# Optimization experiments

Hardware: AMD Instinct MI355X
Metric: run time of the kernel (lower is better)

Reference implementation:

```python
import jax, jax.numpy as jnp
import numpy as np

N = 8192
IN_F = 256
OUT_F = 128
E = 262144
NEG = -9e15


def setup_inputs() -> dict:
    key = jax.random.key(0)
    ks = jax.random.split(key, 12)
    glorot = lambda k, shp: jax.random.uniform(k, shp, jnp.float32,
                                               -jnp.sqrt(6.0 / (shp[0] + shp[1])),
                                               jnp.sqrt(6.0 / (shp[0] + shp[1])))
    return {
        "h_context": jax.random.normal(ks[0], (N, IN_F), jnp.float32),
        "h_structure": jax.random.normal(ks[1], (N, IN_F), jnp.float32),
        "edge_index": jax.random.randint(ks[2], (2, E), 0, N, jnp.int64),
        "Wc_w": glorot(ks[3], (OUT_F, IN_F)),
        "Wc_b": jnp.zeros((OUT_F,), jnp.float32),
        "Ws_w": glorot(ks[4], (OUT_F, IN_F)),
        "Ws_b": jnp.zeros((OUT_F,), jnp.float32),
        "ac_w": glorot(ks[5], (1, 2 * OUT_F)),
        "as_w": glorot(ks[6], (1, 2 * OUT_F)),
        "Ws_coff": jax.random.normal(ks[7], (1, 1), jnp.float32) * 1.414,
        "Wc_coff": jax.random.normal(ks[8], (1, 1), jnp.float32) * 1.414,
    }


def _pair_scores(h, a_w):
    # GAT trick: score[i,j] = leaky_relu(a1 . h[i] + a2 . h[j])
    F_out = h.shape[1]
    s_src = h @ a_w[0, :F_out]   # [N]
    s_dst = h @ a_w[0, F_out:]   # [N]
    return jax.nn.leaky_relu(s_src[:, None] + s_dst[None, :], 0.01)  # [N, N]


def reference(h_context, h_structure, edge_index, Wc_w, Wc_b, Ws_w, Ws_b,
              ac_w, as_w, Ws_coff, Wc_coff):
    hc = h_context @ Wc_w.T + Wc_b                      # [N, F]
    alpha_c = _pair_scores(hc, ac_w)                    # [N, N]
    hs = jax.nn.softmax(h_structure, axis=1) @ Ws_w.T + Ws_b
    alpha_s = _pair_scores(hs, as_w)                    # [N, N]
    alpha = jnp.abs(Ws_coff[0, 0]) * alpha_c + jnp.abs(Wc_coff[0, 0]) * alpha_s
    n = h_structure.shape[0]
    adj = jnp.zeros((n, n), bool).at[edge_index[0], edge_index[1]].set(True)
    attention = jnp.where(adj, alpha, NEG)
    attention = jax.nn.softmax(attention, axis=1)
    # dropout omitted (eval mode / deterministic reference)
    return attention @ hc
```

## Files before the change

kernel.cpp:

```cpp
#include <hip/hip_runtime.h>
#include <math.h>

#define N_NODES 8192
#define IN_FEAT 256
#define OUT_FEAT 128
#define CAP 128
#define M_TILE 32
#define NF_BLOCKS 512

typedef unsigned long long u64;
typedef float v4f __attribute__((ext_vector_type(4)));
typedef short s8v __attribute__((ext_vector_type(8)));
typedef short s4v __attribute__((ext_vector_type(4)));

__device__ __forceinline__ float wred_sum_b(float v) {
    #pragma unroll
    for (int o = 32; o > 0; o >>= 1) v += __shfl_xor(v, o, 64);
    return v;
}
__device__ __forceinline__ float wred_max_b(float v) {
    #pragma unroll
    for (int o = 32; o > 0; o >>= 1) v = fmaxf(v, __shfl_xor(v, o, 64));
    return v;
}

__device__ __forceinline__ void bsplit(float x, unsigned short& hi, unsigned short& lo) {
    unsigned int xb = __float_as_uint(x);
    hi = (unsigned short)(xb >> 16);
    float lof = x - __uint_as_float(xb & 0xFFFF0000u);
    lo = (unsigned short)(__float_as_uint(lof) >> 16);
}

__global__ __launch_bounds__(256) void prep(
    const float* __restrict__ Wc, const float* __restrict__ Ws,
    int* __restrict__ cnt,
    unsigned short* __restrict__ cfrag, unsigned short* __restrict__ sfrag)
{
    int tid = blockIdx.x * 256 + threadIdx.x;
    if (tid < 2048) ((int4*)cnt)[tid] = make_int4(0, 0, 0, 0);

    int mat = tid >> 13;
    int f = tid & 8191;
    int lnf = f & 63;
    int sel = (f >> 6) & 3;
    int ks  = (f >> 8) & 7;
    int wv  = (f >> 11) & 3;
    int row = (wv << 5) + ((sel >> 1) << 4) + (lnf & 15);
    int part = sel & 1;
    int k0 = (ks << 5) + ((lnf >> 4) << 3);
    const float* src = (mat ? Ws : Wc) + row * IN_FEAT + k0;
    short tmp[8];
    #pragma unroll
    for (int j = 0; j < 8; j++) {
        float x = src[j];
        unsigned int xb = __float_as_uint(x);
        if (part == 0) tmp[j] = (short)(xb >> 16);
        else {
            float lof = x - __uint_as_float(xb & 0xFFFF0000u);
            tmp[j] = (short)(__float_as_uint(lof) >> 16);
        }
    }
    unsigned short* dst = (mat ? sfrag : cfrag) + (size_t)f * 8;
    *(s8v*)dst = *(const s8v*)tmp;
}

__global__ __launch_bounds__(256, 4) void node_feats(
    const float* __restrict__ hctx, const float* __restrict__ hstr,
    const unsigned short* __restrict__ cfrag, const unsigned short* __restrict__ sfrag,
    const float* __restrict__ Wcb, const float* __restrict__ Wsb,
    const float* __restrict__ acw, const float* __restrict__ asw,
    const int* __restrict__ ei, int E,
    int* __restrict__ cnt, unsigned short* __restrict__ adj,
    float* __restrict__ hc,
    float* __restrict__ csrc, float* __restrict__ ssrc,
    float* __restrict__ dpack)
{
    __shared__ unsigned short aH[M_TILE][264], aL[M_TILE][264];
    __shared__ float invsh[M_TILE];
    float (*hT)[132] = (float(*)[132])&aH[0][0];

    const int t = threadIdx.x;
    const int w = t >> 6, ln = t & 63;
    const int is_struct = (blockIdx.x >= 256);
    const int b = blockIdx.x & 255;
    const int r0 = b * M_TILE;

    {
        int pv = ei[2 * (ln & 31) + 1];
        u64 nz = __ballot(pv != 0);
        if (nz == 0) {
            for (int e2 = (blockIdx.x * 256 + t) * 2; e2 < E; e2 += NF_BLOCKS * 512) {
                int4 sv = *(const int4*)(ei + 2 * e2);
                int4 dv = *(const int4*)(ei + 2 * E + 2 * e2);
                if ((unsigned)sv.x < N_NODES && (unsigned)dv.x < N_NODES) {
                    int idx = atomicAdd(&cnt[sv.x], 1);
                    if (idx < CAP) adj[(size_t)sv.x * CAP + idx] = (unsigned short)dv.x;
                }
                if (e2 + 1 < E && (unsigned)sv.z < N_NODES && (unsigned)dv.z < N_NODES) {
                    int idx = atomicAdd(&cnt[sv.z], 1);
                    if (idx < CAP) adj[(size_t)sv.z * CAP + idx] = (unsigned short)dv.z;
                }
            }
        } else {
            for (int e = blockIdx.x * 256 + t; e < E; e += NF_BLOCKS * 256) {
                int s = ei[e], d = ei[E + e];
                if ((unsigned)s < N_NODES && (unsigned)d < N_NODES) {
                    int idx = atomicAdd(&cnt[s], 1);
                    if (idx < CAP) adj[(size_t)s * CAP + idx] = (unsigned short)d;
                }
            }
        }
    }

    if (!is_struct) {
        #pragma unroll
        for (int j = 0; j < 8; j++) {
            int c = t + 256 * j;
            int r = c >> 6;
            int k = (c & 63) * 4;
            const float4 x = *(const float4*)(hctx + (size_t)(r0 + r) * IN_FEAT + k);
            unsigned short h0, h1, h2, h3, l0, l1, l2, l3;
            bsplit(x.x, h0, l0); bsplit(x.y, h1, l1);
            bsplit(x.z, h2, l2); bsplit(x.w, h3, l3);
            s4v hv = { (short)h0, (short)h1, (short)h2, (short)h3 };
            s4v lv = { (short)l0, (short)l1, (short)l2, (short)l3 };
            *(s4v*)&aH[r][k] = hv;
            *(s4v*)&aL[r][k] = lv;
        }
    } else {
        #pragma unroll
        for (int rr = 0; rr < 8; rr++) {
            int r = w * 8 + rr;
            const float* srow = hstr + (size_t)(r0 + r) * IN_FEAT;
            float x0 = srow[ln], x1 = srow[ln + 64], x2 = srow[ln + 128], x3 = srow[ln + 192];
            float mx = wred_max_b(fmaxf(fmaxf(x0, x1), fmaxf(x2, x3)));
            float e0 = __expf(x0 - mx), e1 = __expf(x1 - mx);
            float e2 = __expf(x2 - mx), e3 = __expf(x3 - mx);
            float s = wred_sum_b(e0 + e1 + e2 + e3);
            if (ln == 0) invsh[r] = 1.0f / s;
            unsigned short h, l;
            bsplit(e0, h, l); aH[r][ln]       = h; aL[r][ln]       = l;
            bsplit(e1, h, l); aH[r][ln + 64]  = h; aL[r][ln + 64]  = l;
            bsplit(e2, h, l); aH[r][ln + 128] = h; aL[r][ln + 128] = l;
            bsplit(e3, h, l); aH[r][ln + 192] = h; aL[r][ln + 192] = l;
        }
    }
    __syncthreads();

    const int m = ln & 15, q = ln >> 4;
    const unsigned short* frag = is_struct ? sfrag : cfrag;

    v4f a00 = {0.f,0.f,0.f,0.f}, a01 = {0.f,0.f,0.f,0.f};
    v4f a10 = {0.f,0.f,0.f,0.f}, a11 = {0.f,0.f,0.f,0.f};

    #pragma unroll 2
    for (int ks = 0; ks < 8; ks++) {
        const int k0 = ks * 32 + q * 8;
        const s8v* base = (const s8v*)frag + ((w * 8 + ks) * 4) * 64 + ln;
        s8v bh0 = base[0];
        s8v bl0 = base[64];
        s8v bh1 = base[128];
        s8v bl1 = base[192];
        s8v ah0 = *(const s8v*)&aH[m][k0];
        s8v al0 = *(const s8v*)&aL[m][k0];
        s8v ah1 = *(const s8v*)&aH[m + 16][k0];
        s8v al1 = *(const s8v*)&aL[m + 16][k0];
        a00 = __builtin_amdgcn_mfma_f32_16x16x32_bf16(al0, bh0, a00, 0, 0, 0);
        a00 = __builtin_amdgcn_mfma_f32_16x16x32_bf16(ah0, bl0, a00, 0, 0, 0);
        a00 = __builtin_amdgcn_mfma_f32_16x16x32_bf16(ah0, bh0, a00, 0, 0, 0);
        a01 = __builtin_amdgcn_mfma_f32_16x16x32_bf16(al0, bh1, a01, 0, 0, 0);
        a01 = __builtin_amdgcn_mfma_f32_16x16x32_bf16(ah0, bl1, a01, 0, 0, 0);
        a01 = __builtin_amdgcn_mfma_f32_16x16x32_bf16(ah0, bh1, a01, 0, 0, 0);
        a10 = __builtin_amdgcn_mfma_f32_16x16x32_bf16(al1, bh0, a10, 0, 0, 0);
        a10 = __builtin_amdgcn_mfma_f32_16x16x32_bf16(ah1, bl0, a10, 0, 0, 0);
        a10 = __builtin_amdgcn_mfma_f32_16x16x32_bf16(ah1, bh0, a10, 0, 0, 0);
        a11 = __builtin_amdgcn_mfma_f32_16x16x32_bf16(al1, bh1, a11, 0, 0, 0);
        a11 = __builtin_amdgcn_mfma_f32_16x16x32_bf16(ah1, bl1, a11, 0, 0, 0);
        a11 = __builtin_amdgcn_mfma_f32_16x16x32_bf16(ah1, bh1, a11, 0, 0, 0);
    }
    __syncthreads();

    const int nA = (w << 5) + m, nB = nA + 16;
    if (!is_struct) {
        const float bA = Wcb[nA], bB = Wcb[nB];
        #pragma unroll
        for (int p = 0; p < 4; p++) {
            int row = q * 4 + p;
            hT[row][nA]      = a00[p] + bA;
            hT[row][nB]      = a01[p] + bB;
            hT[row + 16][nA] = a10[p] + bA;
            hT[row + 16][nB] = a11[p] + bB;
        }
        __syncthreads();

        #pragma unroll
        for (int j = 0; j < 16; j++) {
            int f = t + 256 * j;
            int r = f >> 7, c = f & 127;
            hc[(size_t)(r0 + r) * OUT_FEAT + c] = hT[r][c];
        }
        float a0 = acw[ln], a0b = acw[ln + 64], a1 = acw[128 + ln], a1b = acw[192 + ln];
        #pragma unroll
        for (int rr = 0; rr < 8; rr++) {
            int r = w * 8 + rr;
            float c0 = hT[r][ln], c1 = hT[r][ln + 64];
            float v0 = wred_sum_b(c0 * a0 + c1 * a0b);
            float v1 = wred_sum_b(c0 * a1 + c1 * a1b);
            if (ln == 0) { csrc[r0 + r] = v0; dpack[2 * (r0 + r)] = v1; }
        }
    } else {
        const float bA = Wsb[nA], bB = Wsb[nB];
        float iv0[4], iv1[4];
        #pragma unroll
        for (int p = 0; p < 4; p++) { iv0[p] = invsh[q * 4 + p]; iv1[p] = invsh[q * 4 + p + 16]; }
        #pragma unroll
        for (int p = 0; p < 4; p++) {
            int row = q * 4 + p;
            hT[row][nA]      = a00[p] * iv0[p] + bA;
            hT[row][nB]      = a01[p] * iv0[p] + bB;
            hT[row + 16][nA] = a10[p] * iv1[p] + bA;
            hT[row + 16][nB] = a11[p] * iv1[p] + bB;
        }
        __syncthreads();

        float b0 = asw[ln], b0b = asw[ln + 64], b1 = asw[128 + ln], b1b = asw[192 + ln];
        #pragma unroll
        for (int rr = 0; rr < 8; rr++) {
            int r = w * 8 + rr;
            float s0 = hT[r][ln], s1 = hT[r][ln + 64];
            float v2 = wred_sum_b(s0 * b0 + s1 * b0b);
            float v3 = wred_sum_b(s0 * b1 + s1 * b1b);
            if (ln == 0) { ssrc[r0 + r] = v2; dpack[2 * (r0 + r) + 1] = v3; }
        }
    }
}

__global__ __launch_bounds__(256) void attn(
    const int* __restrict__ cntArr, const unsigned short* __restrict__ adj,
    const float* __restrict__ hc,
    const float* __restrict__ csrc, const float* __restrict__ ssrc,
    const float2* __restrict__ dpack,
    const float* __restrict__ wscoff, const float* __restrict__ wccoff,
    float* __restrict__ out)
{
    __shared__ float2       jp[4][CAP];
    __shared__ unsigned int bm[4][256];

    const int w  = threadIdx.x >> 6;
    const int ln = threadIdx.x & 63;
    const int i  = blockIdx.x * 4 + w;

    const float wS = fabsf(wscoff[0]);
    const float wC = fabsf(wccoff[0]);
    const float cs = csrc[i], ss = ssrc[i];

    int cnt = cntArr[i];
    if (cnt > CAP) cnt = CAP;

    if (cnt == 0) {
        float2 acc = {0.f, 0.f};
        const float2* hc2f = (const float2*)hc;
        for (int j = 0; j < N_NODES; j++) {
            float2 h2 = hc2f[(size_t)j * 64 + ln];
            acc.x += h2.x; acc.y += h2.y;
        }
        float2 o2 = { acc.x / (float)N_NODES, acc.y / (float)N_NODES };
        *(float2*)(out + (size_t)i * OUT_FEAT + 2 * ln) = o2;
        return;
    }

    bm[w][ln]       = 0u;
    bm[w][ln + 64]  = 0u;
    bm[w][ln + 128] = 0u;
    bm[w][ln + 192] = 0u;

    const unsigned short* row = adj + (size_t)i * CAP;
    int j0 = (ln < cnt)      ? (int)row[ln]      : -1;
    int j1 = (64 + ln < cnt) ? (int)row[64 + ln] : -1;
    __threadfence_block();

    bool keep0 = false, keep1 = false;
    if (j0 >= 0) {
        unsigned int bit = 1u << (j0 & 31);
        keep0 = !(atomicOr(&bm[w][j0 >> 5], bit) & bit);
    }
    if (j1 >= 0) {
        unsigned int bit = 1u << (j1 & 31);
        keep1 = !(atomicOr(&bm[w][j1 >> 5], bit) & bit);
    }

    float al0 = -3e38f, al1 = -3e38f;
    if (keep0) {
        float2 d  = dpack[j0];
        float ac  = cs + d.x;
        float as_ = ss + d.y;
        ac  = (ac  > 0.0f) ? ac  : 0.01f * ac;
        as_ = (as_ > 0.0f) ? as_ : 0.01f * as_;
        al0 = wS * ac + wC * as_;
    }
    if (keep1) {
        float2 d  = dpack[j1];
        float ac  = cs + d.x;
        float as_ = ss + d.y;
        ac  = (ac  > 0.0f) ? ac  : 0.01f * ac;
        as_ = (as_ > 0.0f) ? as_ : 0.01f * as_;
        al1 = wS * ac + wC * as_;
    }

    float m = wred_max_b(fmaxf(al0, al1));
    float p0 = __expf(al0 - m);
    float p1 = __expf(al1 - m);
    float s = wred_sum_b(p0 + p1);
    float inv = 1.0f / s;

    jp[w][ln]      = make_float2(p0, __int_as_float(j0));
    jp[w][64 + ln] = make_float2(p1, __int_as_float(j1));
    __threadfence_block();

    const int half = ln >> 5;
    const int c4   = ln & 31;
    const float4* hc4 = (const float4*)hc;
    float4 acc = {0.f, 0.f, 0.f, 0.f};

    int k = 0;
    for (; k + 8 <= cnt; k += 8) {
        float4 hx[4];
        float  px[4];
        #pragma unroll
        for (int u = 0; u < 4; u++) {
            int idx = k + 2 * u + half;
            float2 e = jp[w][idx];
            px[u] = e.x;
            hx[u] = hc4[__float_as_int(e.y) * 32 + c4];
        }
        #pragma unroll
        for (int u = 0; u < 4; u++) {
            acc.x += px[u] * hx[u].x;
            acc.y += px[u] * hx[u].y;
            acc.z += px[u] * hx[u].z;
            acc.w += px[u] * hx[u].w;
        }
    }
    for (; k < cnt; k += 2) {
        int idx = k + half;
        float2 e = jp[w][(idx < cnt) ? idx : 0];
        float p = (idx < cnt) ? e.x : 0.0f;
        float4 h = hc4[__float_as_int(e.y) * 32 + c4];
        acc.x += p * h.x; acc.y += p * h.y;
        acc.z += p * h.z; acc.w += p * h.w;
    }

    acc.x += __shfl_xor(acc.x, 32, 64);
    acc.y += __shfl_xor(acc.y, 32, 64);
    acc.z += __shfl_xor(acc.z, 32, 64);
    acc.w += __shfl_xor(acc.w, 32, 64);
    if (half == 0) {
        float4 o4 = { acc.x * inv, acc.y * inv, acc.z * inv, acc.w * inv };
        *(float4*)(out + (size_t)i * OUT_FEAT + 4 * c4) = o4;
    }
}

extern "C" void kernel_launch(void* const* d_in, const int* in_sizes, int n_in,
                              void* d_out, int out_size, void* d_ws, size_t ws_size,
                              hipStream_t stream)
{
    const float* hctx = (const float*)d_in[0];
    const float* hstr = (const float*)d_in[1];
    const int*   ei   = (const int*)d_in[2];
    const float* Wc   = (const float*)d_in[3];
    const float* Wcb  = (const float*)d_in[4];
    const float* Ws   = (const float*)d_in[5];
    const float* Wsb  = (const float*)d_in[6];
    const float* acw  = (const float*)d_in[7];
    const float* asw  = (const float*)d_in[8];
    const float* wsco = (const float*)d_in[9];
    const float* wcco = (const float*)d_in[10];
    float* out = (float*)d_out;

    const int n2 = in_sizes[2];
    const int E  = (n2 == 4 * 262144) ? 262144 : n2 / 2;

    char* ws = (char*)d_ws;
    size_t off = 0;
    float* hc    = (float*)(ws + off); off += (size_t)N_NODES * OUT_FEAT * sizeof(float);
    float* csrc  = (float*)(ws + off); off += (size_t)N_NODES * sizeof(float);
    float* ssrc  = (float*)(ws + off); off += (size_t)N_NODES * sizeof(float);
    float* dpack = (float*)(ws + off); off += (size_t)N_NODES * 2 * sizeof(float);
    off = (off + 255) & ~(size_t)255;
    int* cnt = (int*)(ws + off);      off += (size_t)N_NODES * sizeof(int);
    unsigned short* adj = (unsigned short*)(ws + off); off += (size_t)N_NODES * CAP * sizeof(unsigned short);
    unsigned short* cfrag = (unsigned short*)(ws + off); off += (size_t)8192 * 8 * sizeof(unsigned short);
    unsigned short* sfrag = (unsigned short*)(ws + off); off += (size_t)8192 * 8 * sizeof(unsigned short);

    prep<<<64, 256, 0, stream>>>(Wc, Ws, cnt, cfrag, sfrag);
    node_feats<<<NF_BLOCKS, 256, 0, stream>>>(hctx, hstr, cfrag, sfrag, Wcb, Wsb,
                                              acw, asw, ei, E, cnt, adj,
                                              hc, csrc, ssrc, dpack);
    attn<<<N_NODES / 4, 256, 0, stream>>>(cnt, adj, hc, csrc, ssrc, (const float2*)dpack,
                                          wsco, wcco, out);
}
```

Before: 116.9 us.

## Fuse prep, node features and attention into one cooperative kernel with grid syncs

```diff
diff --git a/kernel.cpp b/kernel.cpp
--- a/kernel.cpp
+++ b/kernel.cpp
@@ -1,12 +1,14 @@
 #include <hip/hip_runtime.h>
+#include <hip/hip_cooperative_groups.h>
 #include <math.h>
+
+namespace cg = cooperative_groups;
 
 #define N_NODES 8192
 #define IN_FEAT 256
 #define OUT_FEAT 128
 #define CAP 128
 #define M_TILE 32
-#define NF_BLOCKS 512
 
 typedef unsigned long long u64;
 typedef float v4f __attribute__((ext_vector_type(4)));
@@ -31,65 +33,64 @@
     lo = (unsigned short)(__float_as_uint(lof) >> 16);
 }
 
-__global__ __launch_bounds__(256) void prep(
+__device__ __forceinline__ void dev_prep(int tid,
     const float* __restrict__ Wc, const float* __restrict__ Ws,
     int* __restrict__ cnt,
     unsigned short* __restrict__ cfrag, unsigned short* __restrict__ sfrag)
 {
-    int tid = blockIdx.x * 256 + threadIdx.x;
     if (tid < 2048) ((int4*)cnt)[tid] = make_int4(0, 0, 0, 0);
-
-    int mat = tid >> 13;
-    int f = tid & 8191;
-    int lnf = f & 63;
-    int sel = (f >> 6) & 3;
-    int ks  = (f >> 8) & 7;
-    int wv  = (f >> 11) & 3;
-    int row = (wv << 5) + ((sel >> 1) << 4) + (lnf & 15);
-    int part = sel & 1;
-    int k0 = (ks << 5) + ((lnf >> 4) << 3);
-    const float* src = (mat ? Ws : Wc) + row * IN_FEAT + k0;
-    short tmp[8];
-    #pragma unroll
-    for (int j = 0; j < 8; j++) {
-        float x = src[j];
-        unsigned int xb = __float_as_uint(x);
-        if (part == 0) tmp[j] = (short)(xb >> 16);
-        else {
-            float lof = x - __uint_as_float(xb & 0xFFFF0000u);
-            tmp[j] = (short)(__float_as_uint(lof) >> 16);
-        }
-    }
-    unsigned short* dst = (mat ? sfrag : cfrag) + (size_t)f * 8;
-    *(s8v*)dst = *(const s8v*)tmp;
-}
-
-__global__ __launch_bounds__(256, 4) void node_feats(
+    if (tid < 16384) {
+        int mat = tid >> 13;
+        int f = tid & 8191;
+        int lnf = f & 63;
+        int sel = (f >> 6) & 3;
+        int ks  = (f >> 8) & 7;
+        int wv  = (f >> 11) & 3;
+        int row = (wv << 5) + ((sel >> 1) << 4) + (lnf & 15);
+        int part = sel & 1;
+        int k0 = (ks << 5) + ((lnf >> 4) << 3);
+        const float* src = (mat ? Ws : Wc) + row * IN_FEAT + k0;
+        short tmp[8];
+        #pragma unroll
+        for (int j = 0; j < 8; j++) {
+            float x = src[j];
+            unsigned int xb = __float_as_uint(x);
+            if (part == 0) tmp[j] = (short)(xb >> 16);
+            else {
+                float lof = x - __uint_as_float(xb & 0xFFFF0000u);
+                tmp[j] = (short)(__float_as_uint(lof) >> 16);
+            }
+        }
+        unsigned short* dst = (mat ? sfrag : cfrag) + (size_t)f * 8;
+        *(s8v*)dst = *(const s8v*)tmp;
+    }
+}
+
+__device__ __forceinline__ void dev_nf(
     const float* __restrict__ hctx, const float* __restrict__ hstr,
     const unsigned short* __restrict__ cfrag, const unsigned short* __restrict__ sfrag,
     const float* __restrict__ Wcb, const float* __restrict__ Wsb,
     const float* __restrict__ acw, const float* __restrict__ asw,
     const int* __restrict__ ei, int E,
     int* __restrict__ cnt, unsigned short* __restrict__ adj,
-    float* __restrict__ hc,
-    float* __restrict__ csrc, float* __restrict__ ssrc,
-    float* __restrict__ dpack)
-{
-    __shared__ unsigned short aH[M_TILE][264], aL[M_TILE][264];
+    float* __restrict__ hc, float* __restrict__ csrc, float* __restrict__ ssrc,
+    float* __restrict__ dpack, int blk, int t)
+{
+    __shared__ __align__(16) unsigned short aH[M_TILE][264], aL[M_TILE][264];
     __shared__ float invsh[M_TILE];
     float (*hT)[132] = (float(*)[132])&aH[0][0];
 
-    const int t = threadIdx.x;
     const int w = t >> 6, ln = t & 63;
-    const int is_struct = (blockIdx.x >= 256);
-    const int b = blockIdx.x & 255;
+    const int is_struct = (blk >= 256);
+    const int b = blk & 255;
     const int r0 = b * M_TILE;
 
-    {
+    if (!is_struct) {
         int pv = ei[2 * (ln & 31) + 1];
         u64 nz = __ballot(pv != 0);
+        int ctid = blk * 512 + t;
         if (nz == 0) {
-            for (int e2 = (blockIdx.x * 256 + t) * 2; e2 < E; e2 += NF_BLOCKS * 512) {
+            for (int e2 = ctid * 2; e2 < E; e2 += 262144) {
                 int4 sv = *(const int4*)(ei + 2 * e2);
                 int4 dv = *(const int4*)(ei + 2 * E + 2 * e2);
                 if ((unsigned)sv.x < N_NODES && (unsigned)dv.x < N_NODES) {
@@ -102,7 +103,7 @@
                 }
             }
         } else {
-            for (int e = blockIdx.x * 256 + t; e < E; e += NF_BLOCKS * 256) {
+            for (int e = ctid; e < E; e += 131072) {
                 int s = ei[e], d = ei[E + e];
                 if ((unsigned)s < N_NODES && (unsigned)d < N_NODES) {
                     int idx = atomicAdd(&cnt[s], 1);
@@ -110,12 +111,9 @@
                 }
             }
         }
-    }
-
-    if (!is_struct) {
-        #pragma unroll
-        for (int j = 0; j < 8; j++) {
-            int c = t + 256 * j;
+        #pragma unroll
+        for (int j = 0; j < 4; j++) {
+            int c = t + 512 * j;
             int r = c >> 6;
             int k = (c & 63) * 4;
             const float4 x = *(const float4*)(hctx + (size_t)(r0 + r) * IN_FEAT + k);
@@ -129,8 +127,8 @@
         }
     } else {
         #pragma unroll
-        for (int rr = 0; rr < 8; rr++) {
-            int r = w * 8 + rr;
+        for (int rr = 0; rr < 4; rr++) {
+            int r = w * 4 + rr;
             const float* srow = hstr + (size_t)(r0 + r) * IN_FEAT;
             float x0 = srow[ln], x1 = srow[ln + 64], x2 = srow[ln + 128], x3 = srow[ln + 192];
             float mx = wred_max_b(fmaxf(fmaxf(x0, x1), fmaxf(x2, x3)));
@@ -148,85 +146,71 @@
     __syncthreads();
 
     const int m = ln & 15, q = ln >> 4;
+    const int w4 = w >> 1, pair = w & 1;
     const unsigned short* frag = is_struct ? sfrag : cfrag;
 
-    v4f a00 = {0.f,0.f,0.f,0.f}, a01 = {0.f,0.f,0.f,0.f};
-    v4f a10 = {0.f,0.f,0.f,0.f}, a11 = {0.f,0.f,0.f,0.f};
+    v4f a00 = {0.f,0.f,0.f,0.f}, a10 = {0.f,0.f,0.f,0.f};
 
     #pragma unroll 2
     for (int ks = 0; ks < 8; ks++) {
         const int k0 = ks * 32 + q * 8;
-        const s8v* base = (const s8v*)frag + ((w * 8 + ks) * 4) * 64 + ln;
-        s8v bh0 = base[0];
-        s8v bl0 = base[64];
-        s8v bh1 = base[128];
-        s8v bl1 = base[192];
+        const s8v* base = (const s8v*)frag + ((w4 * 8 + ks) * 4) * 64 + pair * 128 + ln;
+        s8v bh = base[0];
+        s8v bl = base[64];
         s8v ah0 = *(const s8v*)&aH[m][k0];
         s8v al0 = *(const s8v*)&aL[m][k0];
         s8v ah1 = *(const s8v*)&aH[m + 16][k0];
         s8v al1 = *(const s8v*)&aL[m + 16][k0];
-        a00 = __builtin_amdgcn_mfma_f32_16x16x32_bf16(al0, bh0, a00, 0, 0, 0);
-        a00 = __builtin_amdgcn_mfma_f32_16x16x32_bf16(ah0, bl0, a00, 0, 0, 0);
-        a00 = __builtin_amdgcn_mfma_f32_16x16x32_bf16(ah0, bh0, a00, 0, 0, 0);
-        a01 = __builtin_amdgcn_mfma_f32_16x16x32_bf16(al0, bh1, a01, 0, 0, 0);
-        a01 = __builtin_amdgcn_mfma_f32_16x16x32_bf16(ah0, bl1, a01, 0, 0, 0);
-        a01 = __builtin_amdgcn_mfma_f32_16x16x32_bf16(ah0, bh1, a01, 0, 0, 0);
-        a10 = __builtin_amdgcn_mfma_f32_16x16x32_bf16(al1, bh0, a10, 0, 0, 0);
-        a10 = __builtin_amdgcn_mfma_f32_16x16x32_bf16(ah1, bl0, a10, 0, 0, 0);
-        a10 = __builtin_amdgcn_mfma_f32_16x16x32_bf16(ah1, bh0, a10, 0, 0, 0);
-        a11 = __builtin_amdgcn_mfma_f32_16x16x32_bf16(al1, bh1, a11, 0, 0, 0);
-        a11 = __builtin_amdgcn_mfma_f32_16x16x32_bf16(ah1, bl1, a11, 0, 0, 0);
-        a11 = __builtin_amdgcn_mfma_f32_16x16x32_bf16(ah1, bh1, a11, 0, 0, 0);
+        a00 = __builtin_amdgcn_mfma_f32_16x16x32_bf16(al0, bh, a00, 0, 0, 0);
+        a00 = __builtin_amdgcn_mfma_f32_16x16x32_bf16(ah0, bl, a00, 0, 0, 0);
+        a00 = __builtin_amdgcn_mfma_f32_16x16x32_bf16(ah0, bh, a00, 0, 0, 0);
+        a10 = __builtin_amdgcn_mfma_f32_16x16x32_bf16(al1, bh, a10, 0, 0, 0);
+        a10 = __builtin_amdgcn_mfma_f32_16x16x32_bf16(ah1, bl, a10, 0, 0, 0);
+        a10 = __builtin_amdgcn_mfma_f32_16x16x32_bf16(ah1, bh, a10, 0, 0, 0);
     }
     __syncthreads();
 
-    const int nA = (w << 5) + m, nB = nA + 16;
+    const int nc = (w << 4) + m;
     if (!is_struct) {
-        const float bA = Wcb[nA], bB = Wcb[nB];
+        const float bC = Wcb[nc];
         #pragma unroll
         for (int p = 0; p < 4; p++) {
             int row = q * 4 + p;
-            hT[row][nA]      = a00[p] + bA;
-            hT[row][nB]      = a01[p] + bB;
-            hT[row + 16][nA] = a10[p] + bA;
-            hT[row + 16][nB] = a11[p] + bB;
+            hT[row][nc]      = a00[p] + bC;
+            hT[row + 16][nc] = a10[p] + bC;
         }
         __syncthreads();
-
-        #pragma unroll
-        for (int j = 0; j < 16; j++) {
-            int f = t + 256 * j;
-            int r = f >> 7, c = f & 127;
-            hc[(size_t)(r0 + r) * OUT_FEAT + c] = hT[r][c];
+        #pragma unroll
+        for (int j = 0; j < 8; j++) {
+            int f = t + 512 * j;
+            int r = f >> 7, c2 = f & 127;
+            hc[(size_t)(r0 + r) * OUT_FEAT + c2] = hT[r][c2];
         }
         float a0 = acw[ln], a0b = acw[ln + 64], a1 = acw[128 + ln], a1b = acw[192 + ln];
         #pragma unroll
-        for (int rr = 0; rr < 8; rr++) {
-            int r = w * 8 + rr;
+        for (int rr = 0; rr < 4; rr++) {
+            int r = w * 4 + rr;
             float c0 = hT[r][ln], c1 = hT[r][ln + 64];
             float v0 = wred_sum_b(c0 * a0 + c1 * a0b);
             float v1 = wred_sum_b(c0 * a1 + c1 * a1b);
             if (ln == 0) { csrc[r0 + r] = v0; dpack[2 * (r0 + r)] = v1; }
         }
     } else {
-        const float bA = Wsb[nA], bB = Wsb[nB];
+        const float bS = Wsb[nc];
         float iv0[4], iv1[4];
         #pragma unroll
         for (int p = 0; p < 4; p++) { iv0[p] = invsh[q * 4 + p]; iv1[p] = invsh[q * 4 + p + 16]; }
         #pragma unroll
         for (int p = 0; p < 4; p++) {
             int row = q * 4 + p;
-            hT[row][nA]      = a00[p] * iv0[p] + bA;
-            hT[row][nB]      = a01[p] * iv0[p] + bB;
-            hT[row + 16][nA] = a10[p] * iv1[p] + bA;
-            hT[row + 16][nB] = a11[p] * iv1[p] + bB;
+            hT[row][nc]      = a00[p] * iv0[p] + bS;
+            hT[row + 16][nc] = a10[p] * iv1[p] + bS;
         }
         __syncthreads();
-
         float b0 = asw[ln], b0b = asw[ln + 64], b1 = asw[128 + ln], b1b = asw[192 + ln];
         #pragma unroll
-        for (int rr = 0; rr < 8; rr++) {
-            int r = w * 8 + rr;
+        for (int rr = 0; rr < 4; rr++) {
+            int r = w * 4 + rr;
             float s0 = hT[r][ln], s1 = hT[r][ln + 64];
             float v2 = wred_sum_b(s0 * b0 + s1 * b0b);
             float v3 = wred_sum_b(s0 * b1 + s1 * b1b);
@@ -235,25 +219,14 @@
     }
 }
 
-__global__ __launch_bounds__(256) void attn(
+__device__ __forceinline__ void dev_attn_row(int i, int ln,
+    float2* jp, unsigned int* bm,
     const int* __restrict__ cntArr, const unsigned short* __restrict__ adj,
-    const float* __restrict__ hc,
-    const float* __restrict__ csrc, const float* __restrict__ ssrc,
-    const float2* __restrict__ dpack,
-    const float* __restrict__ wscoff, const float* __restrict__ wccoff,
-    float* __restrict__ out)
-{
-    __shared__ float2       jp[4][CAP];
-    __shared__ unsigned int bm[4][256];
-
-    const int w  = threadIdx.x >> 6;
-    const int ln = threadIdx.x & 63;
-    const int i  = blockIdx.x * 4 + w;
-
-    const float wS = fabsf(wscoff[0]);
-    const float wC = fabsf(wccoff[0]);
+    const float* __restrict__ hc, const float* __restrict__ csrc,
+    const float* __restrict__ ssrc, const float2* __restrict__ dpack,
+    float wS, float wC, float* __restrict__ out)
+{
     const float cs = csrc[i], ss = ssrc[i];
-
     int cnt = cntArr[i];
     if (cnt > CAP) cnt = CAP;
 
@@ -269,10 +242,7 @@
         return;
     }
 
-    bm[w][ln]       = 0u;
-    bm[w][ln + 64]  = 0u;
-    bm[w][ln + 128] = 0u;
-    bm[w][ln + 192] = 0u;
+    bm[ln] = 0u; bm[ln + 64] = 0u; bm[ln + 128] = 0u; bm[ln + 192] = 0u;
 
     const unsigned short* row = adj + (size_t)i * CAP;
     int j0 = (ln < cnt)      ? (int)row[ln]      : -1;
@@ -282,11 +252,11 @@
     bool keep0 = false, keep1 = false;
     if (j0 >= 0) {
         unsigned int bit = 1u << (j0 & 31);
-        keep0 = !(atomicOr(&bm[w][j0 >> 5], bit) & bit);
+        keep0 = !(atomicOr(&bm[j0 >> 5], bit) & bit);
     }
     if (j1 >= 0) {
         unsigned int bit = 1u << (j1 & 31);
-        keep1 = !(atomicOr(&bm[w][j1 >> 5], bit) & bit);
+        keep1 = !(atomicOr(&bm[j1 >> 5], bit) & bit);
     }
 
     float al0 = -3e38f, al1 = -3e38f;
@@ -307,14 +277,14 @@
         al1 = wS * ac + wC * as_;
     }
 
-    float m = wred_max_b(fmaxf(al0, al1));
-    float p0 = __expf(al0 - m);
-    float p1 = __expf(al1 - m);
+    float mm = wred_max_b(fmaxf(al0, al1));
+    float p0 = __expf(al0 - mm);
+    float p1 = __expf(al1 - mm);
     float s = wred_sum_b(p0 + p1);
     float inv = 1.0f / s;
 
-    jp[w][ln]      = make_float2(p0, __int_as_float(j0));
-    jp[w][64 + ln] = make_float2(p1, __int_as_float(j1));
+    jp[ln]      = make_float2(p0, __int_as_float(j0));
+    jp[64 + ln] = make_float2(p1, __int_as_float(j1));
     __threadfence_block();
 
     const int half = ln >> 5;
@@ -329,7 +299,7 @@
         #pragma unroll
         for (int u = 0; u < 4; u++) {
             int idx = k + 2 * u + half;
-            float2 e = jp[w][idx];
+            float2 e = jp[idx];
             px[u] = e.x;
             hx[u] = hc4[__float_as_int(e.y) * 32 + c4];
         }
@@ -343,7 +313,7 @@
     }
     for (; k < cnt; k += 2) {
         int idx = k + half;
-        float2 e = jp[w][(idx < cnt) ? idx : 0];
+        float2 e = jp[(idx < cnt) ? idx : 0];
         float p = (idx < cnt) ? e.x : 0.0f;
         float4 h = hc4[__float_as_int(e.y) * 32 + c4];
         acc.x += p * h.x; acc.y += p * h.y;
@@ -358,6 +328,64 @@
         float4 o4 = { acc.x * inv, acc.y * inv, acc.z * inv, acc.w * inv };
         *(float4*)(out + (size_t)i * OUT_FEAT + 4 * c4) = o4;
     }
+}
+
+struct FA {
+    const float *hctx, *hstr, *Wc, *Ws, *Wcb, *Wsb, *acw, *asw;
+    const int *ei;
+    int E;
+    const float *wsco, *wcco;
+    int *cnt;
+    unsigned short *adj;
+    float *hc, *csrc, *ssrc, *dpack;
+    unsigned short *cfrag, *sfrag;
+    float *out;
+};
+
+__global__ __launch_bounds__(512, 4) void fused(FA a)
+{
+    const int t = threadIdx.x, blk = blockIdx.x;
+    dev_prep(blk * 512 + t, a.Wc, a.Ws, a.cnt, a.cfrag, a.sfrag);
+    cg::this_grid().sync();
+    dev_nf(a.hctx, a.hstr, a.cfrag, a.sfrag, a.Wcb, a.Wsb, a.acw, a.asw,
+           a.ei, a.E, a.cnt, a.adj, a.hc, a.csrc, a.ssrc, a.dpack, blk, t);
+    cg::this_grid().sync();
+
+    __shared__ __align__(16) float2 jpA[8][CAP];
+    __shared__ unsigned int bmA[8][256];
+    const int w = t >> 6, ln = t & 63;
+    const float wS  = fabsf(a.wsco[0]);
+    const float wCc = fabsf(a.wcco[0]);
+    dev_attn_row(blk * 16 + w * 2,     ln, &jpA[w][0], &bmA[w][0], a.cnt, a.adj,
+                 a.hc, a.csrc, a.ssrc, (const float2*)a.dpack, wS, wCc, a.out);
+    dev_attn_row(blk * 16 + w * 2 + 1, ln, &jpA[w][0], &bmA[w][0], a.cnt, a.adj,
+                 a.hc, a.csrc, a.ssrc, (const float2*)a.dpack, wS, wCc, a.out);
+}
+
+__global__ __launch_bounds__(256) void prep_k(
+    const float* __restrict__ Wc, const float* __restrict__ Ws,
+    int* __restrict__ cnt,
+    unsigned short* __restrict__ cfrag, unsigned short* __restrict__ sfrag)
+{
+    dev_prep(blockIdx.x * 256 + threadIdx.x, Wc, Ws, cnt, cfrag, sfrag);
+}
+
+__global__ __launch_bounds__(512, 4) void nf_k(FA a)
+{
+    dev_nf(a.hctx, a.hstr, a.cfrag, a.sfrag, a.Wcb, a.Wsb, a.acw, a.asw,
+           a.ei, a.E, a.cnt, a.adj, a.hc, a.csrc, a.ssrc, a.dpack,
+           blockIdx.x, threadIdx.x);
+}
+
+__global__ __launch_bounds__(256) void attn_k(FA a)
+{
+    __shared__ __align__(16) float2 jpA[4][CAP];
+    __shared__ unsigned int bmA[4][256];
+    const int w = threadIdx.x >> 6, ln = threadIdx.x & 63;
+    const float wS  = fabsf(a.wsco[0]);
+    const float wCc = fabsf(a.wcco[0]);
+    dev_attn_row(blockIdx.x * 4 + w, ln, &jpA[w][0], &bmA[w][0], a.cnt, a.adj,
+                 a.hc, a.csrc, a.ssrc, (const float2*)a.dpack, wS, wCc, a.out);
 }
 
 extern "C" void kernel_launch(void* const* d_in, const int* in_sizes, int n_in,
@@ -378,7 +406,7 @@
     float* out = (float*)d_out;
 
     const int n2 = in_sizes[2];
-    const int E  = (n2 == 4 * 262144) ? 262144 : n2 / 2;
+    int E = (n2 == 4 * 262144) ? 262144 : n2 / 2;
 
     char* ws = (char*)d_ws;
     size_t off = 0;
@@ -392,10 +420,20 @@
     unsigned short* cfrag = (unsigned short*)(ws + off); off += (size_t)8192 * 8 * sizeof(unsigned short);
     unsigned short* sfrag = (unsigned short*)(ws + off); off += (size_t)8192 * 8 * sizeof(unsigned short);
 
-    prep<<<64, 256, 0, stream>>>(Wc, Ws, cnt, cfrag, sfrag);
-    node_feats<<<NF_BLOCKS, 256, 0, stream>>>(hctx, hstr, cfrag, sfrag, Wcb, Wsb,
-                                              acw, asw, ei, E, cnt, adj,
-                                              hc, csrc, ssrc, dpack);
-    attn<<<N_NODES / 4, 256, 0, stream>>>(cnt, adj, hc, csrc, ssrc, (const float2*)dpack,
-                                          wsco, wcco, out);
-}
+    FA fa;
+    fa.hctx = hctx; fa.hstr = hstr; fa.Wc = Wc; fa.Ws = Ws;
+    fa.Wcb = Wcb; fa.Wsb = Wsb; fa.acw = acw; fa.asw = asw;
+    fa.ei = ei; fa.E = E; fa.wsco = wsco; fa.wcco = wcco;
+    fa.cnt = cnt; fa.adj = adj; fa.hc = hc; fa.csrc = csrc; fa.ssrc = ssrc;
+    fa.dpack = dpack; fa.cfrag = cfrag; fa.sfrag = sfrag; fa.out = out;
+
+    void* args[] = { (void*)&fa };
+    hipError_t ce = hipLaunchCooperativeKernel(fused, dim3(512), dim3(512),
+                                               args, 0, stream);
+    if (ce != hipSuccess) {
+        (void)hipGetLastError();
+        prep_k<<<64, 256, 0, stream>>>(Wc, Ws, cnt, cfrag, sfrag);
+        nf_k<<<512, 512, 0, stream>>>(fa);
+        attn_k<<<N_NODES / 4, 256, 0, stream>>>(fa);
+    }
+}
```

Measured after the change: 241.6 us. +106.8%, slower.

## Double node-feature block size and move edge scatter to context blocks only

Applied to the files above, without the earlier changes.

```diff
diff --git a/kernel.cpp b/kernel.cpp
--- a/kernel.cpp
+++ b/kernel.cpp
@@ -6,7 +6,6 @@
 #define OUT_FEAT 128
 #define CAP 128
 #define M_TILE 32
-#define NF_BLOCKS 512
 
 typedef unsigned long long u64;
 typedef float v4f __attribute__((ext_vector_type(4)));
@@ -31,7 +30,7 @@
     lo = (unsigned short)(__float_as_uint(lof) >> 16);
 }
 
-__global__ __launch_bounds__(256) void prep(
+__global__ __launch_bounds__(256) void prep_k(
     const float* __restrict__ Wc, const float* __restrict__ Ws,
     int* __restrict__ cnt,
     unsigned short* __restrict__ cfrag, unsigned short* __restrict__ sfrag)
@@ -64,32 +63,32 @@
     *(s8v*)dst = *(const s8v*)tmp;
 }
 
-__global__ __launch_bounds__(256, 4) void node_feats(
+__global__ __launch_bounds__(512, 4) void nf_k(
     const float* __restrict__ hctx, const float* __restrict__ hstr,
     const unsigned short* __restrict__ cfrag, const unsigned short* __restrict__ sfrag,
     const float* __restrict__ Wcb, const float* __restrict__ Wsb,
     const float* __restrict__ acw, const float* __restrict__ asw,
     const int* __restrict__ ei, int E,
     int* __restrict__ cnt, unsigned short* __restrict__ adj,
-    float* __restrict__ hc,
-    float* __restrict__ csrc, float* __restrict__ ssrc,
+    float* __restrict__ hc, float* __restrict__ csrc, float* __restrict__ ssrc,
     float* __restrict__ dpack)
 {
-    __shared__ unsigned short aH[M_TILE][264], aL[M_TILE][264];
+    __shared__ __align__(16) unsigned short aH[M_TILE][264], aL[M_TILE][264];
     __shared__ float invsh[M_TILE];
     float (*hT)[132] = (float(*)[132])&aH[0][0];
 
-    const int t = threadIdx.x;
+    const int t = threadIdx.x, blk = blockIdx.x;
     const int w = t >> 6, ln = t & 63;
-    const int is_struct = (blockIdx.x >= 256);
-    const int b = blockIdx.x & 255;
+    const int is_struct = (blk >= 256);
+    const int b = blk & 255;
     const int r0 = b * M_TILE;
 
-    {
+    if (!is_struct) {
         int pv = ei[2 * (ln & 31) + 1];
         u64 nz = __ballot(pv != 0);
+        int ctid = blk * 512 + t;
         if (nz == 0) {
-            for (int e2 = (blockIdx.x * 256 + t) * 2; e2 < E; e2 += NF_BLOCKS * 512) {
+            for (int e2 = ctid * 2; e2 < E; e2 += 262144) {
                 int4 sv = *(const int4*)(ei + 2 * e2);
                 int4 dv = *(const int4*)(ei + 2 * E + 2 * e2);
                 if ((unsigned)sv.x < N_NODES && (unsigned)dv.x < N_NODES) {
@@ -102,7 +101,7 @@
                 }
             }
         } else {
-            for (int e = blockIdx.x * 256 + t; e < E; e += NF_BLOCKS * 256) {
+            for (int e = ctid; e < E; e += 131072) {
                 int s = ei[e], d = ei[E + e];
                 if ((unsigned)s < N_NODES && (unsigned)d < N_NODES) {
                     int idx = atomicAdd(&cnt[s], 1);
@@ -110,12 +109,9 @@
                 }
             }
         }
-    }
-
-    if (!is_struct) {
-        #pragma unroll
-        for (int j = 0; j < 8; j++) {
-            int c = t + 256 * j;
+        #pragma unroll
+        for (int j = 0; j < 4; j++) {
+            int c = t + 512 * j;
             int r = c >> 6;
             int k = (c & 63) * 4;
             const float4 x = *(const float4*)(hctx + (size_t)(r0 + r) * IN_FEAT + k);
@@ -129,8 +125,8 @@
         }
     } else {
         #pragma unroll
-        for (int rr = 0; rr < 8; rr++) {
-            int r = w * 8 + rr;
+        for (int rr = 0; rr < 4; rr++) {
+            int r = w * 4 + rr;
             const float* srow = hstr + (size_t)(r0 + r) * IN_FEAT;
             float x0 = srow[ln], x1 = srow[ln + 64], x2 = srow[ln + 128], x3 = srow[ln + 192];
             float mx = wred_max_b(fmaxf(fmaxf(x0, x1), fmaxf(x2, x3)));
@@ -148,85 +144,71 @@
     __syncthreads();
 
     const int m = ln & 15, q = ln >> 4;
+    const int w4 = w >> 1, pair = w & 1;
     const unsigned short* frag = is_struct ? sfrag : cfrag;
 
-    v4f a00 = {0.f,0.f,0.f,0.f}, a01 = {0.f,0.f,0.f,0.f};
-    v4f a10 = {0.f,0.f,0.f,0.f}, a11 = {0.f,0.f,0.f,0.f};
+    v4f a00 = {0.f,0.f,0.f,0.f}, a10 = {0.f,0.f,0.f,0.f};
 
     #pragma unroll 2
     for (int ks = 0; ks < 8; ks++) {
         const int k0 = ks * 32 + q * 8;
-        const s8v* base = (const s8v*)frag + ((w * 8 + ks) * 4) * 64 + ln;
-        s8v bh0 = base[0];
-        s8v bl0 = base[64];
-        s8v bh1 = base[128];
-        s8v bl1 = base[192];
+        const s8v* base = (const s8v*)frag + ((w4 * 8 + ks) * 4) * 64 + pair * 128 + ln;
+        s8v bh = base[0];
+        s8v bl = base[64];
         s8v ah0 = *(const s8v*)&aH[m][k0];
         s8v al0 = *(const s8v*)&aL[m][k0];
         s8v ah1 = *(const s8v*)&aH[m + 16][k0];
         s8v al1 = *(const s8v*)&aL[m + 16][k0];
-        a00 = __builtin_amdgcn_mfma_f32_16x16x32_bf16(al0, bh0, a00, 0, 0, 0);
-        a00 = __builtin_amdgcn_mfma_f32_16x16x32_bf16(ah0, bl0, a00, 0, 0, 0);
-        a00 = __builtin_amdgcn_mfma_f32_16x16x32_bf16(ah0, bh0, a00, 0, 0, 0);
-        a01 = __builtin_amdgcn_mfma_f32_16x16x32_bf16(al0, bh1, a01, 0, 0, 0);
-        a01 = __builtin_amdgcn_mfma_f32_16x16x32_bf16(ah0, bl1, a01, 0, 0, 0);
-        a01 = __builtin_amdgcn_mfma_f32_16x16x32_bf16(ah0, bh1, a01, 0, 0, 0);
-        a10 = __builtin_amdgcn_mfma_f32_16x16x32_bf16(al1, bh0, a10, 0, 0, 0);
-        a10 = __builtin_amdgcn_mfma_f32_16x16x32_bf16(ah1, bl0, a10, 0, 0, 0);
-        a10 = __builtin_amdgcn_mfma_f32_16x16x32_bf16(ah1, bh0, a10, 0, 0, 0);
-        a11 = __builtin_amdgcn_mfma_f32_16x16x32_bf16(al1, bh1, a11, 0, 0, 0);
-        a11 = __builtin_amdgcn_mfma_f32_16x16x32_bf16(ah1, bl1, a11, 0, 0, 0);
-        a11 = __builtin_amdgcn_mfma_f32_16x16x32_bf16(ah1, bh1, a11, 0, 0, 0);
+        a00 = __builtin_amdgcn_mfma_f32_16x16x32_bf16(al0, bh, a00, 0, 0, 0);
+        a00 = __builtin_amdgcn_mfma_f32_16x16x32_bf16(ah0, bl, a00, 0, 0, 0);
+        a00 = __builtin_amdgcn_mfma_f32_16x16x32_bf16(ah0, bh, a00, 0, 0, 0);
+        a10 = __builtin_amdgcn_mfma_f32_16x16x32_bf16(al1, bh, a10, 0, 0, 0);
+        a10 = __builtin_amdgcn_mfma_f32_16x16x32_bf16(ah1, bl, a10, 0, 0, 0);
+        a10 = __builtin_amdgcn_mfma_f32_16x16x32_bf16(ah1, bh, a10, 0, 0, 0);
     }
     __syncthreads();
 
-    const int nA = (w << 5) + m, nB = nA + 16;
+    const int nc = (w << 4) + m;
     if (!is_struct) {
-        const float bA = Wcb[nA], bB = Wcb[nB];
+        const float bC = Wcb[nc];
         #pragma unroll
         for (int p = 0; p < 4; p++) {
             int row = q * 4 + p;
-            hT[row][nA]      = a00[p] + bA;
-            hT[row][nB]      = a01[p] + bB;
-            hT[row + 16][nA] = a10[p] + bA;
-            hT[row + 16][nB] = a11[p] + bB;
+            hT[row][nc]      = a00[p] + bC;
+            hT[row + 16][nc] = a10[p] + bC;
         }
         __syncthreads();
-
-        #pragma unroll
-        for (int j = 0; j < 16; j++) {
-            int f = t + 256 * j;
-            int r = f >> 7, c = f & 127;
-            hc[(size_t)(r0 + r) * OUT_FEAT + c] = hT[r][c];
+        #pragma unroll
+        for (int j = 0; j < 8; j++) {
+            int f = t + 512 * j;
+            int r = f >> 7, c2 = f & 127;
+            hc[(size_t)(r0 + r) * OUT_FEAT + c2] = hT[r][c2];
         }
         float a0 = acw[ln], a0b = acw[ln + 64], a1 = acw[128 + ln], a1b = acw[192 + ln];
         #pragma unroll
-        for (int rr = 0; rr < 8; rr++) {
-            int r = w * 8 + rr;
+        for (int rr = 0; rr < 4; rr++) {
+            int r = w * 4 + rr;
             float c0 = hT[r][ln], c1 = hT[r][ln + 64];
             float v0 = wred_sum_b(c0 * a0 + c1 * a0b);
             float v1 = wred_sum_b(c0 * a1 + c1 * a1b);
             if (ln == 0) { csrc[r0 + r] = v0; dpack[2 * (r0 + r)] = v1; }
         }
     } else {
-        const float bA = Wsb[nA], bB = Wsb[nB];
+        const float bS = Wsb[nc];
         float iv0[4], iv1[4];
         #pragma unroll
         for (int p = 0; p < 4; p++) { iv0[p] = invsh[q * 4 + p]; iv1[p] = invsh[q * 4 + p + 16]; }
         #pragma unroll
         for (int p = 0; p < 4; p++) {
             int row = q * 4 + p;
-            hT[row][nA]      = a00[p] * iv0[p] + bA;
-            hT[row][nB]      = a01[p] * iv0[p] + bB;
-            hT[row + 16][nA] = a10[p] * iv1[p] + bA;
-            hT[row + 16][nB] = a11[p] * iv1[p] + bB;
+            hT[row][nc]      = a00[p] * iv0[p] + bS;
+            hT[row + 16][nc] = a10[p] * iv1[p] + bS;
         }
         __syncthreads();
-
         float b0 = asw[ln], b0b = asw[ln + 64], b1 = asw[128 + ln], b1b = asw[192 + ln];
         #pragma unroll
-        for (int rr = 0; rr < 8; rr++) {
-            int r = w * 8 + rr;
+        for (int rr = 0; rr < 4; rr++) {
+            int r = w * 4 + rr;
             float s0 = hT[r][ln], s1 = hT[r][ln + 64];
             float v2 = wred_sum_b(s0 * b0 + s1 * b0b);
             float v3 = wred_sum_b(s0 * b1 + s1 * b1b);
@@ -235,7 +217,7 @@
     }
 }
 
-__global__ __launch_bounds__(256) void attn(
+__global__ __launch_bounds__(256) void attn_k(
     const int* __restrict__ cntArr, const unsigned short* __restrict__ adj,
     const float* __restrict__ hc,
     const float* __restrict__ csrc, const float* __restrict__ ssrc,
@@ -243,7 +225,7 @@
     const float* __restrict__ wscoff, const float* __restrict__ wccoff,
     float* __restrict__ out)
 {
-    __shared__ float2       jp[4][CAP];
+    __shared__ __align__(16) float2 jp[4][CAP];
     __shared__ unsigned int bm[4][256];
 
     const int w  = threadIdx.x >> 6;
@@ -392,10 +374,11 @@
     unsigned short* cfrag = (unsigned short*)(ws + off); off += (size_t)8192 * 8 * sizeof(unsigned short);
     unsigned short* sfrag = (unsigned short*)(ws + off); off += (size_t)8192 * 8 * sizeof(unsigned short);
 
-    prep<<<64, 256, 0, stream>>>(Wc, Ws, cnt, cfrag, sfrag);
-    node_feats<<<NF_BLOCKS, 256, 0, stream>>>(hctx, hstr, cfrag, sfrag, Wcb, Wsb,
-                                              acw, asw, ei, E, cnt, adj,
-                                              hc, csrc, ssrc, dpack);
-    attn<<<N_NODES / 4, 256, 0, stream>>>(cnt, adj, hc, csrc, ssrc, (const float2*)dpack,
-                                          wsco, wcco, out);
-}
+    prep_k<<<64, 256, 0, stream>>>(Wc, Ws, cnt, cfrag, sfrag);
+    nf_k<<<512, 512, 0, stream>>>(hctx, hstr, cfrag, sfrag, Wcb, Wsb,
+                                  acw, asw, ei, E, cnt, adj,
+                                  hc, csrc, ssrc, dpack);
+    attn_k<<<N_NODES / 4, 256, 0, stream>>>(cnt, adj, hc, csrc, ssrc,
+                                            (const float2*)dpack,
+                                            wsco, wcco, out);
+}
```

Result: faster. 111.7 us (-4.4%).
